# Kernel tuning notes

Hardware: AMD Instinct MI355X
Metric: run time of the kernel (lower is better)

## Reference

```python
import jax, jax.numpy as jnp
import numpy as np

N, E, F, H, C, K = 100000, 1600000, 512, 256, 64, 10
EPS = 1e-5  # BatchNorm1d default eps


def setup_inputs() -> dict:
    key = jax.random.key(0)
    ks = jax.random.split(key, 8)
    x = jax.random.normal(ks[0], (N, F), jnp.float32)
    # edge list with no self-loops (gcn_norm adds the self-loops itself)
    src = jax.random.randint(ks[1], (E,), 0, N)
    off = jax.random.randint(ks[2], (E,), 1, N)
    dst = (src + off) % N
    edge_index = jnp.stack([src, dst])
    s = lambda k, sh: jax.random.normal(k, sh, jnp.float32) * 0.02
    W0 = s(ks[3], (F, H)); b0 = jnp.zeros((H,), jnp.float32)
    g0 = jnp.ones((H,), jnp.float32); be0 = jnp.zeros((H,), jnp.float32)
    W1 = s(ks[4], (H, H)); b1 = jnp.zeros((H,), jnp.float32)
    g1 = jnp.ones((H,), jnp.float32); be1 = jnp.zeros((H,), jnp.float32)
    W2 = s(ks[5], (H, C)); b2 = jnp.zeros((C,), jnp.float32)
    proj_w = s(ks[6], (C, 1)); proj_b = jnp.zeros((1,), jnp.float32)
    return dict(x=x, W0=W0, b0=b0, g0=g0, be0=be0, W1=W1, b1=b1, g1=g1,
                be1=be1, W2=W2, b2=b2, proj_w=proj_w, proj_b=proj_b,
                edge_index=edge_index)


def _batchnorm(h, gamma, beta):
    # training-mode BN over the node (batch) axis, biased variance like torch
    mu = h.mean(0)
    var = h.var(0)
    return gamma * (h - mu) * jax.lax.rsqrt(var + EPS) + beta


def _prop(x, edge_index, proj_w, proj_b):
    n, c = x.shape
    loop = jnp.arange(n, dtype=edge_index.dtype)
    row = jnp.concatenate([edge_index[0], loop])  # message sources (x_j)
    col = jnp.concatenate([edge_index[1], loop])  # aggregation targets
    w = jnp.ones(row.shape, x.dtype)
    deg = jax.ops.segment_sum(w, col, num_segments=n)
    dis = jnp.where(deg > 0, jax.lax.rsqrt(jnp.maximum(deg, 1.0)) * (deg > 0), 0.0)
    dis = jnp.where(deg > 0, deg ** -0.5, 0.0)
    norm = dis[row] * dis[col]  # symmetric GCN normalization per edge

    def hop(xk, _):
        msgs = norm[:, None] * xk[row]               # gather + scale  [E+N, C]
        xk = jax.ops.segment_sum(msgs, col, num_segments=n)  # scatter-add
        return xk, xk

    _, hops = jax.lax.scan(hop, x, None, length=K)   # [K, N, C]
    pps = jnp.concatenate([x[None], hops], axis=0).transpose(1, 0, 2)  # [N, K+1, C]
    score = jax.nn.sigmoid(pps @ proj_w + proj_b)[..., 0]  # [N, K+1]
    return jnp.einsum('nk,nkc->nc', score, pps)      # [N, C]


def reference(x, W0, b0, g0, be0, W1, b1, g1, be1, W2, b2, proj_w, proj_b,
              edge_index):
    h = jax.nn.relu(_batchnorm(x @ W0 + b0, g0, be0))   # dropout is identity (eval)
    h = jax.nn.relu(_batchnorm(h @ W1 + b1, g1, be1))
    h = h @ W2 + b2                                     # [N, C] logits
    out = _prop(h, edge_index, proj_w, proj_b)
    return jax.nn.log_softmax(out, axis=1)
```

## Files before the change

### kernel.cpp

```cpp
#include <hip/hip_runtime.h>
#include <hip/hip_bf16.h>
#include <math.h>

#define NN 100000
#define FF 512
#define HH 256
#define CC 64
#define KHOPS 10
#define BN_EPS 1e-5f

typedef __bf16 bf16x8 __attribute__((ext_vector_type(8)));
typedef float f32x4 __attribute__((ext_vector_type(4)));
typedef unsigned short ushort8v __attribute__((ext_vector_type(8)));

__device__ __forceinline__ unsigned short f2bf(float f) {
    __bf16 b = (__bf16)f;
    return __builtin_bit_cast(unsigned short, b);
}
__device__ __forceinline__ float bf2f(unsigned short h) {
    unsigned u = ((unsigned)h) << 16;
    return __builtin_bit_cast(float, u);
}
__device__ __forceinline__ float lo16(unsigned u) { return bf2f((unsigned short)(u & 0xFFFF)); }
__device__ __forceinline__ float hi16(unsigned u) { return bf2f((unsigned short)(u >> 16)); }
__device__ __forceinline__ unsigned pk(float a, float b) {
    return ((unsigned)f2bf(b) << 16) | (unsigned)f2bf(a);
}

typedef __attribute__((address_space(1))) const void g_void;
typedef __attribute__((address_space(3))) void l_void;
__device__ __forceinline__ void gl2lds16(const void* g, void* l) {
    __builtin_amdgcn_global_load_lds((g_void*)g, (l_void*)l, 16, 0, 0);
}

__global__ void k_zero(float* p, int n) {
    int i = blockIdx.x * blockDim.x + threadIdx.x;
    if (i < n) p[i] = 0.f;
}

__global__ void k_deg_init(int* deg, int n) {
    int i = blockIdx.x * blockDim.x + threadIdx.x;
    if (i < n) deg[i] = 1;
}

__global__ void k_deg_count(const int* __restrict__ dst, int e, int* deg) {
    for (int i = blockIdx.x * blockDim.x + threadIdx.x; i < e; i += gridDim.x * blockDim.x)
        atomicAdd(&deg[dst[i]], 1);
}

__global__ void k_dis(const int* __restrict__ deg, float* dis, int n) {
    int i = blockIdx.x * blockDim.x + threadIdx.x;
    if (i < n) dis[i] = rsqrtf((float)deg[i]);
}

#define SCAN_B 1024
#define SCAN_NB ((NN + SCAN_B - 1) / SCAN_B)

__global__ void k_scan1(const int* __restrict__ deg, int* __restrict__ part, int n) {
    __shared__ int ls[SCAN_B];
    int i = blockIdx.x * SCAN_B + threadIdx.x;
    ls[threadIdx.x] = (i < n) ? deg[i] - 1 : 0;
    __syncthreads();
    for (int d = SCAN_B / 2; d > 0; d >>= 1) {
        if (threadIdx.x < d) ls[threadIdx.x] += ls[threadIdx.x + d];
        __syncthreads();
    }
    if (threadIdx.x == 0) part[blockIdx.x] = ls[0];
}

__global__ void k_scan2(int* part, int* offs_last, int nb) {
    if (threadIdx.x == 0) {
        int run = 0;
        for (int b = 0; b < nb; b++) { int v = part[b]; part[b] = run; run += v; }
        offs_last[0] = run;
    }
}

__global__ void k_scan3(const int* __restrict__ deg, const int* __restrict__ part,
                        int* __restrict__ offs, int* __restrict__ cur, int n) {
    __shared__ int ls[SCAN_B];
    int i = blockIdx.x * SCAN_B + threadIdx.x;
    int v = (i < n) ? deg[i] - 1 : 0;
    ls[threadIdx.x] = v;
    __syncthreads();
    for (int d = 1; d < SCAN_B; d <<= 1) {
        int t = (threadIdx.x >= d) ? ls[threadIdx.x - d] : 0;
        __syncthreads();
        ls[threadIdx.x] += t;
        __syncthreads();
    }
    if (i < n) {
        int ex = part[blockIdx.x] + ls[threadIdx.x] - v;
        offs[i] = ex;
        cur[i] = ex;
    }
}

__global__ void k_fill(const int* __restrict__ src, const int* __restrict__ dst, int e,
                       const float* __restrict__ dis, int* cursor,
                       int* __restrict__ csrc, float* __restrict__ cw) {
    for (int i = blockIdx.x * blockDim.x + threadIdx.x; i < e; i += gridDim.x * blockDim.x) {
        int d = dst[i];
        int s = src[i];
        int p = atomicAdd(&cursor[d], 1);
        csrc[p] = s;
        cw[p] = dis[s] * dis[d];
    }
}

__global__ void k_wt(const float* __restrict__ W, unsigned short* __restrict__ Wt,
                     int K, int N) {
    int i = blockIdx.x * blockDim.x + threadIdx.x;
    if (i < K * N) {
        int n = i / K;
        int k = i - n * K;
        Wt[i] = f2bf(W[(size_t)k * N + n]);
    }
}

template <int AF32, int BN_, int STATS, int NW>
__global__ __launch_bounds__(NW * 64) void k_gemm_mfma(
    const void* __restrict__ Av, const unsigned short* __restrict__ Bt,
    const float* __restrict__ bias, unsigned short* __restrict__ Cb,
    float* __restrict__ sum, float* __restrict__ sumsq,
    int M, int K, int Nd) {
    constexpr int NT = NW * 64;
    constexpr int WC = (NW == 8) ? 4 : 2;
    constexpr int PWN = BN_ / WC;
    constexpr int NREP = PWN / 16;
    constexpr int ACH = AF32 ? 8 : 4;
    constexpr int AOPS = 128 * ACH / NT;
    constexpr int BOPS = BN_ * 4 / NT;
    constexpr int ASZ = AF32 ? 16384 : 8192;
    __shared__ __align__(16) unsigned char Asb[ASZ];
    __shared__ __align__(16) unsigned char Bsb[BN_ * 64];
    const int tid = threadIdx.x;
    const int lane = tid & 63;
    const int wid = tid >> 6;
    const int wrow = wid / WC, wcol = wid % WC;
    const int row_base = blockIdx.y * 128;
    const int col_base = blockIdx.x * BN_;
    const unsigned char* Abase = (const unsigned char*)Av;
    const size_t arowb = (size_t)K * (AF32 ? 4 : 2);

    f32x4 acc[4][NREP];
#pragma unroll
    for (int m = 0; m < 4; m++)
#pragma unroll
        for (int n = 0; n < NREP; n++)
#pragma unroll
            for (int j = 0; j < 4; j++) acc[m][n][j] = 0.f;

    for (int kt = 0; kt < K; kt += 32) {
#pragma unroll
        for (int i = 0; i < AOPS; ++i) {
            int e = i * NT + tid;
            int r = e / ACH;
            int c = e % ACH;
            int cs = AF32 ? (c ^ (r & 7)) : (c ^ ((r >> 1) & 3));
            int grow = row_base + r;
            if (grow > M - 1) grow = M - 1;
            const void* g = Abase + (size_t)grow * arowb + (size_t)kt * (AF32 ? 4 : 2) + (cs << 4);
            gl2lds16(g, Asb + e * 16);
        }
#pragma unroll
        for (int i = 0; i < BOPS; ++i) {
            int e = i * NT + tid;
            int r = e >> 2, c = e & 3;
            int cs = c ^ ((r >> 1) & 3);
            const void* g = (const unsigned char*)Bt + (size_t)(col_base + r) * (K * 2) +
                            (size_t)kt * 2 + (cs << 4);
            gl2lds16(g, Bsb + e * 16);
        }
        __syncthreads();

        bf16x8 af[4], bfr[NREP];
#pragma unroll
        for (int m = 0; m < 4; ++m) {
            int r = wrow * 64 + m * 16 + (lane & 15);
            if (AF32) {
                int x7 = r & 7;
                int q2 = (lane >> 4) * 2;
                f32x4 f0 = *(const f32x4*)(Asb + r * 128 + ((q2 ^ x7) << 4));
                f32x4 f1 = *(const f32x4*)(Asb + r * 128 + (((q2 + 1) ^ x7) << 4));
                bf16x8 a;
                a[0] = (__bf16)f0[0]; a[1] = (__bf16)f0[1]; a[2] = (__bf16)f0[2]; a[3] = (__bf16)f0[3];
                a[4] = (__bf16)f1[0]; a[5] = (__bf16)f1[1]; a[6] = (__bf16)f1[2]; a[7] = (__bf16)f1[3];
                af[m] = a;
            } else {
                int cs = (lane >> 4) ^ ((r >> 1) & 3);
                af[m] = *(const bf16x8*)(Asb + r * 64 + (cs << 4));
            }
        }
#pragma unroll
        for (int n = 0; n < NREP; ++n) {
            int r = wcol * PWN + n * 16 + (lane & 15);
            int cs = (lane >> 4) ^ ((r >> 1) & 3);
            bfr[n] = *(const bf16x8*)(Bsb + r * 64 + (cs << 4));
        }
#pragma unroll
        for (int m = 0; m < 4; ++m)
#pragma unroll
            for (int n = 0; n < NREP; ++n)
                acc[m][n] = __builtin_amdgcn_mfma_f32_16x16x32_bf16(af[m], bfr[n], acc[m][n], 0, 0, 0);
        __syncthreads();
    }

    const int lc = lane & 15;
    const int lr = (lane >> 4) * 4;
#pragma unroll
    for (int m = 0; m < 4; ++m) {
        int gr0 = row_base + wrow * 64 + m * 16 + lr;
#pragma unroll
        for (int n = 0; n < NREP; ++n) {
            int gc = col_base + wcol * PWN + n * 16 + lc;
            float bb = bias[gc];
#pragma unroll
            for (int j = 0; j < 4; ++j) {
                int gr = gr0 + j;
                if (gr < M) Cb[(size_t)gr * Nd + gc] = f2bf(acc[m][n][j] + bb);
            }
        }
    }
    if (STATS) {
#pragma unroll
        for (int n = 0; n < NREP; ++n) {
            int gc = col_base + wcol * PWN + n * 16 + lc;
            float bb = bias[gc];
            float s = 0.f, s2 = 0.f;
#pragma unroll
            for (int m = 0; m < 4; ++m) {
                int gr0 = row_base + wrow * 64 + m * 16 + lr;
#pragma unroll
                for (int j = 0; j < 4; ++j) {
                    if (gr0 + j < M) {
                        float v = acc[m][n][j] + bb;
                        s += v;
                        s2 += v * v;
                    }
                }
            }
            s += __shfl_xor(s, 16); s += __shfl_xor(s, 32);
            s2 += __shfl_xor(s2, 16); s2 += __shfl_xor(s2, 32);
            if ((lane >> 4) == 0) {
                atomicAdd(&sum[gc], s);
                atomicAdd(&sumsq[gc], s2);
            }
        }
    }
}

__global__ void k_bnfin(const float* __restrict__ sum, const float* __restrict__ sq,
                        const float* __restrict__ g, const float* __restrict__ be,
                        float* scale, float* shift) {
    int c = threadIdx.x;
    float mu = sum[c] * (1.f / NN);
    float var = sq[c] * (1.f / NN) - mu * mu;
    float sc = g[c] * rsqrtf(var + BN_EPS);
    scale[c] = sc;
    shift[c] = be[c] - mu * sc;
}

__global__ void k_bnapply(unsigned short* __restrict__ h, const float* __restrict__ scale,
                          const float* __restrict__ shift, int n) {
    int total = n * 32;
    for (int idx = blockIdx.x * blockDim.x + threadIdx.x; idx < total;
         idx += gridDim.x * blockDim.x) {
        int c8 = (idx & 31) * 8;
        ushort8v v = *(ushort8v*)(h + (size_t)idx * 8);
        f32x4 s0 = *(const f32x4*)(scale + c8);
        f32x4 s1 = *(const f32x4*)(scale + c8 + 4);
        f32x4 h0 = *(const f32x4*)(shift + c8);
        f32x4 h1 = *(const f32x4*)(shift + c8 + 4);
#pragma unroll
        for (int j = 0; j < 4; j++) {
            v[j] = f2bf(fmaxf(bf2f(v[j]) * s0[j] + h0[j], 0.f));
            v[j + 4] = f2bf(fmaxf(bf2f(v[j + 4]) * s1[j] + h1[j], 0.f));
        }
        *(ushort8v*)(h + (size_t)idx * 8) = v;
    }
}

__global__ void k_hop(const unsigned short* __restrict__ xin,
                      unsigned short* __restrict__ xout,
                      const int* __restrict__ offs, const int* __restrict__ csrc,
                      const float* __restrict__ cw, const float* __restrict__ dis,
                      int n) {
    int wid = (int)((blockIdx.x * (size_t)blockDim.x + threadIdx.x) >> 6);
    if (wid >= n) return;
    int lane = threadIdx.x & 63;
    int g = lane >> 3;
    int j = lane & 7;
    const uint4* x16 = (const uint4*)xin;
    float y0 = 0.f, y1 = 0.f, y2 = 0.f, y3 = 0.f, y4 = 0.f, y5 = 0.f, y6 = 0.f, y7 = 0.f;
    if (g == 0) {
        float dn = dis[wid];
        float w = dn * dn;
        uint4 v = x16[(size_t)wid * 8 + j];
        y0 = w * lo16(v.x); y1 = w * hi16(v.x);
        y2 = w * lo16(v.y); y3 = w * hi16(v.y);
        y4 = w * lo16(v.z); y5 = w * hi16(v.z);
        y6 = w * lo16(v.w); y7 = w * hi16(v.w);
    }
    int p0 = offs[wid], p1 = offs[wid + 1];
    int p = p0 + g;
    for (; p + 8 < p1; p += 16) {
        int sA = csrc[p], sB = csrc[p + 8];
        float wA = cw[p], wB = cw[p + 8];
        uint4 vA = x16[(size_t)sA * 8 + j];
        uint4 vB = x16[(size_t)sB * 8 + j];
        y0 += wA * lo16(vA.x); y1 += wA * hi16(vA.x);
        y2 += wA * lo16(vA.y); y3 += wA * hi16(vA.y);
        y4 += wA * lo16(vA.z); y5 += wA * hi16(vA.z);
        y6 += wA * lo16(vA.w); y7 += wA * hi16(vA.w);
        y0 += wB * lo16(vB.x); y1 += wB * hi16(vB.x);
        y2 += wB * lo16(vB.y); y3 += wB * hi16(vB.y);
        y4 += wB * lo16(vB.z); y5 += wB * hi16(vB.z);
        y6 += wB * lo16(vB.w); y7 += wB * hi16(vB.w);
    }
    for (; p < p1; p += 8) {
        int s = csrc[p];
        float w = cw[p];
        uint4 v = x16[(size_t)s * 8 + j];
        y0 += w * lo16(v.x); y1 += w * hi16(v.x);
        y2 += w * lo16(v.y); y3 += w * hi16(v.y);
        y4 += w * lo16(v.z); y5 += w * hi16(v.z);
        y6 += w * lo16(v.w); y7 += w * hi16(v.w);
    }
#pragma unroll
    for (int m = 8; m <= 32; m <<= 1) {
        y0 += __shfl_xor(y0, m); y1 += __shfl_xor(y1, m);
        y2 += __shfl_xor(y2, m); y3 += __shfl_xor(y3, m);
        y4 += __shfl_xor(y4, m); y5 += __shfl_xor(y5, m);
        y6 += __shfl_xor(y6, m); y7 += __shfl_xor(y7, m);
    }
    if (g == 0) {
        uint4 r;
        r.x = pk(y0, y1); r.y = pk(y2, y3); r.z = pk(y4, y5); r.w = pk(y6, y7);
        ((uint4*)xout)[(size_t)wid * 8 + j] = r;
    }
}

struct XPack { const unsigned short* p[KHOPS + 1]; };

__global__ void k_finprop(XPack xp, const float* __restrict__ pw,
                          const float* __restrict__ pbp, float* __restrict__ out, int n) {
    int gw = (int)((blockIdx.x * (size_t)blockDim.x + threadIdx.x) >> 6);
    int lane = threadIdx.x & 63;
    int hf = lane >> 5;
    int l = lane & 31;
    int node = gw * 2 + hf;
    if (node >= n) return;
    float pw0 = pw[2 * l], pw1 = pw[2 * l + 1];
    float pb0 = pbp[0];
    float o0 = 0.f, o1 = 0.f;
#pragma unroll
    for (int k = 0; k <= KHOPS; k++) {
        unsigned v = ((const unsigned*)xp.p[k])[(size_t)node * 32 + l];
        float v0 = lo16(v);
        float v1 = hi16(v);
        float d = v0 * pw0 + v1 * pw1;
#pragma unroll
        for (int m = 16; m >= 1; m >>= 1) d += __shfl_xor(d, m);
        float s = 1.f / (1.f + expf(-(d + pb0)));
        o0 += s * v0;
        o1 += s * v1;
    }
    float mx = fmaxf(o0, o1);
#pragma unroll
    for (int m = 16; m >= 1; m >>= 1) mx = fmaxf(mx, __shfl_xor(mx, m));
    float e = expf(o0 - mx) + expf(o1 - mx);
#pragma unroll
    for (int m = 16; m >= 1; m >>= 1) e += __shfl_xor(e, m);
    float lg = mx + logf(e);
    float2 r = make_float2(o0 - lg, o1 - lg);
    *(float2*)(out + (size_t)node * 64 + 2 * l) = r;
}

extern "C" void kernel_launch(void* const* d_in, const int* in_sizes, int n_in,
                              void* d_out, int out_size, void* d_ws, size_t ws_size,
                              hipStream_t stream) {
    const float* x  = (const float*)d_in[0];
    const float* W0 = (const float*)d_in[1];
    const float* b0 = (const float*)d_in[2];
    const float* g0 = (const float*)d_in[3];
    const float* be0 = (const float*)d_in[4];
    const float* W1 = (const float*)d_in[5];
    const float* b1 = (const float*)d_in[6];
    const float* g1 = (const float*)d_in[7];
    const float* be1 = (const float*)d_in[8];
    const float* W2 = (const float*)d_in[9];
    const float* b2 = (const float*)d_in[10];
    const float* pw = (const float*)d_in[11];
    const float* pb = (const float*)d_in[12];
    const int* ei = (const int*)d_in[13];
    const int E = in_sizes[13] / 2;
    const int* esrc = ei;
    const int* edst = ei + E;

    char* ws = (char*)d_ws;
    const size_t XKB = (size_t)NN * CC * 2;
    unsigned short* h0b = (unsigned short*)(ws + 0);
    unsigned short* h1b = (unsigned short*)(ws + 51200000);
    unsigned short* xk[KHOPS + 1];
    xk[0] = (unsigned short*)(ws + 0);
    xk[5] = (unsigned short*)(ws + XKB);
    xk[6] = (unsigned short*)(ws + 2 * XKB);
    xk[7] = (unsigned short*)(ws + 3 * XKB);
    xk[1] = (unsigned short*)(ws + 51200000);
    xk[2] = (unsigned short*)(ws + 51200000 + XKB);
    xk[3] = (unsigned short*)(ws + 51200000 + 2 * XKB);
    xk[4] = (unsigned short*)(ws + 51200000 + 3 * XKB);
    xk[8] = (unsigned short*)(ws + 102400000);
    xk[9] = (unsigned short*)(ws + 115200000);
    xk[10] = (unsigned short*)(ws + 128000000);

    int*   deg  = (int*)  (ws + 140800000);
    float* dis  = (float*)(ws + 141200000);
    int*   offs = (int*)  (ws + 141600000);
    int*   cur  = (int*)  (ws + 142000064);
    int*   csrc = (int*)  (ws + 142400064);
    float* cw   = (float*)(ws + 148800064);
    float* stats = (float*)(ws + 155200064);
    int*   part = (int*)  (ws + 155208256);
    unsigned short* W0t = (unsigned short*)(ws + 155209280);
    unsigned short* W1t = (unsigned short*)(ws + 155471424);
    unsigned short* W2t = (unsigned short*)(ws + 155602496);

    float* sum0 = stats,        *sq0 = stats + 256;
    float* sum1 = stats + 512,  *sq1 = stats + 768;
    float* scale0 = stats + 1024, *shift0 = stats + 1280;
    float* scale1 = stats + 1536, *shift1 = stats + 1792;

    float* out = (float*)d_out;

    const int TPB = 256;
    int ngrid = (NN + TPB - 1) / TPB;
    int egrid = (E + TPB - 1) / TPB;
    int wgrid = (NN * 64 + TPB - 1) / TPB;
    int wgrid2 = (((NN + 1) / 2) * 64 + TPB - 1) / TPB;
    int mtiles = (NN + 127) / 128;

    k_zero<<<2, 1024, 0, stream>>>(stats, 2048);
    k_deg_init<<<ngrid, TPB, 0, stream>>>(deg, NN);
    k_deg_count<<<egrid, TPB, 0, stream>>>(edst, E, deg);
    k_dis<<<ngrid, TPB, 0, stream>>>(deg, dis, NN);
    k_scan1<<<SCAN_NB, SCAN_B, 0, stream>>>(deg, part, NN);
    k_scan2<<<1, 64, 0, stream>>>(part, offs + NN, SCAN_NB);
    k_scan3<<<SCAN_NB, SCAN_B, 0, stream>>>(deg, part, offs, cur, NN);
    k_fill<<<egrid, TPB, 0, stream>>>(esrc, edst, E, dis, cur, csrc, cw);

    k_wt<<<(FF * HH + TPB - 1) / TPB, TPB, 0, stream>>>(W0, W0t, FF, HH);
    k_wt<<<(HH * HH + TPB - 1) / TPB, TPB, 0, stream>>>(W1, W1t, HH, HH);
    k_wt<<<(HH * CC + TPB - 1) / TPB, TPB, 0, stream>>>(W2, W2t, HH, CC);

    k_gemm_mfma<1, 256, 1, 8><<<dim3(1, mtiles), 512, 0, stream>>>(
        x, W0t, b0, h0b, sum0, sq0, NN, FF, HH);
    k_bnfin<<<1, 256, 0, stream>>>(sum0, sq0, g0, be0, scale0, shift0);
    k_bnapply<<<2048, TPB, 0, stream>>>(h0b, scale0, shift0, NN);

    k_gemm_mfma<0, 256, 1, 8><<<dim3(1, mtiles), 512, 0, stream>>>(
        h0b, W1t, b1, h1b, sum1, sq1, NN, HH, HH);
    k_bnfin<<<1, 256, 0, stream>>>(sum1, sq1, g1, be1, scale1, shift1);
    k_bnapply<<<2048, TPB, 0, stream>>>(h1b, scale1, shift1, NN);

    k_gemm_mfma<0, 64, 0, 4><<<dim3(1, mtiles), 256, 0, stream>>>(
        h1b, W2t, b2, xk[0], nullptr, nullptr, NN, HH, CC);

    for (int k = 0; k < KHOPS; k++)
        k_hop<<<wgrid, TPB, 0, stream>>>(xk[k], xk[k + 1], offs, csrc, cw, dis, NN);

    XPack xp;
    for (int k = 0; k <= KHOPS; k++) xp.p[k] = xk[k];
    k_finprop<<<wgrid2, TPB, 0, stream>>>(xp, pw, pb, out, NN);
}
```

Baseline: 887.0 us.

## Fuse BatchNorm apply into next GEMM and load operands directly to registers

Removes the two separate BN+ReLU apply passes by applying scale/shift/ReLU to the A operand inside the following GEMM's load path. The GEMM is also restructured to skip LDS staging: each wave loads its A and B fragments straight from global memory into registers, double-buffered across K steps. This saves two full read-write passes over 100k×256 bf16 activations and the LDS barriers. In exchange, B fragments are reloaded redundantly by every wave and A rows are read without LDS sharing, which may increase global and L2 traffic.

```diff
diff --git a/kernel.cpp b/kernel.cpp
--- a/kernel.cpp
+++ b/kernel.cpp
@@ -25,12 +25,6 @@
 __device__ __forceinline__ float hi16(unsigned u) { return bf2f((unsigned short)(u >> 16)); }
 __device__ __forceinline__ unsigned pk(float a, float b) {
     return ((unsigned)f2bf(b) << 16) | (unsigned)f2bf(a);
-}
-
-typedef __attribute__((address_space(1))) const void g_void;
-typedef __attribute__((address_space(3))) void l_void;
-__device__ __forceinline__ void gl2lds16(const void* g, void* l) {
-    __builtin_amdgcn_global_load_lds((g_void*)g, (l_void*)l, 16, 0, 0);
 }
 
 __global__ void k_zero(float* p, int n) {
@@ -118,102 +112,111 @@
     }
 }
 
-template <int AF32, int BN_, int STATS, int NW>
-__global__ __launch_bounds__(NW * 64) void k_gemm_mfma(
+template <int AF32, int WR, int WC, int STATS, int FUSEBN>
+__global__ __launch_bounds__(WR * WC * 64) void k_gemm_direct(
     const void* __restrict__ Av, const unsigned short* __restrict__ Bt,
     const float* __restrict__ bias, unsigned short* __restrict__ Cb,
+    const float* __restrict__ bnscale, const float* __restrict__ bnshift,
     float* __restrict__ sum, float* __restrict__ sumsq,
     int M, int K, int Nd) {
-    constexpr int NT = NW * 64;
-    constexpr int WC = (NW == 8) ? 4 : 2;
-    constexpr int PWN = BN_ / WC;
-    constexpr int NREP = PWN / 16;
-    constexpr int ACH = AF32 ? 8 : 4;
-    constexpr int AOPS = 128 * ACH / NT;
-    constexpr int BOPS = BN_ * 4 / NT;
-    constexpr int ASZ = AF32 ? 16384 : 8192;
-    __shared__ __align__(16) unsigned char Asb[ASZ];
-    __shared__ __align__(16) unsigned char Bsb[BN_ * 64];
     const int tid = threadIdx.x;
     const int lane = tid & 63;
     const int wid = tid >> 6;
     const int wrow = wid / WC, wcol = wid % WC;
-    const int row_base = blockIdx.y * 128;
-    const int col_base = blockIdx.x * BN_;
-    const unsigned char* Abase = (const unsigned char*)Av;
-    const size_t arowb = (size_t)K * (AF32 ? 4 : 2);
-
-    f32x4 acc[4][NREP];
+    const int row0 = blockIdx.y * (WR * 64) + wrow * 64;
+    const int col0 = wcol * 64;
+    const int rl = lane & 15;
+    const int kl = (lane >> 4) * 8;
+    const float* Af = (const float*)Av;
+    const unsigned short* Ab = (const unsigned short*)Av;
+
+    int arow[4];
+#pragma unroll
+    for (int m = 0; m < 4; ++m) {
+        int r = row0 + m * 16 + rl;
+        arow[m] = (r < M) ? r : (M - 1);
+    }
+
+    f32x4 acc[4][4];
 #pragma unroll
     for (int m = 0; m < 4; m++)
 #pragma unroll
-        for (int n = 0; n < NREP; n++)
+        for (int n = 0; n < 4; n++)
 #pragma unroll
             for (int j = 0; j < 4; j++) acc[m][n][j] = 0.f;
 
-    for (int kt = 0; kt < K; kt += 32) {
-#pragma unroll
-        for (int i = 0; i < AOPS; ++i) {
-            int e = i * NT + tid;
-            int r = e / ACH;
-            int c = e % ACH;
-            int cs = AF32 ? (c ^ (r & 7)) : (c ^ ((r >> 1) & 3));
-            int grow = row_base + r;
-            if (grow > M - 1) grow = M - 1;
-            const void* g = Abase + (size_t)grow * arowb + (size_t)kt * (AF32 ? 4 : 2) + (cs << 4);
-            gl2lds16(g, Asb + e * 16);
-        }
-#pragma unroll
-        for (int i = 0; i < BOPS; ++i) {
-            int e = i * NT + tid;
-            int r = e >> 2, c = e & 3;
-            int cs = c ^ ((r >> 1) & 3);
-            const void* g = (const unsigned char*)Bt + (size_t)(col_base + r) * (K * 2) +
-                            (size_t)kt * 2 + (cs << 4);
-            gl2lds16(g, Bsb + e * 16);
-        }
-        __syncthreads();
-
-        bf16x8 af[4], bfr[NREP];
-#pragma unroll
-        for (int m = 0; m < 4; ++m) {
-            int r = wrow * 64 + m * 16 + (lane & 15);
-            if (AF32) {
-                int x7 = r & 7;
-                int q2 = (lane >> 4) * 2;
-                f32x4 f0 = *(const f32x4*)(Asb + r * 128 + ((q2 ^ x7) << 4));
-                f32x4 f1 = *(const f32x4*)(Asb + r * 128 + (((q2 + 1) ^ x7) << 4));
-                bf16x8 a;
-                a[0] = (__bf16)f0[0]; a[1] = (__bf16)f0[1]; a[2] = (__bf16)f0[2]; a[3] = (__bf16)f0[3];
-                a[4] = (__bf16)f1[0]; a[5] = (__bf16)f1[1]; a[6] = (__bf16)f1[2]; a[7] = (__bf16)f1[3];
-                af[m] = a;
-            } else {
-                int cs = (lane >> 4) ^ ((r >> 1) & 3);
-                af[m] = *(const bf16x8*)(Asb + r * 64 + (cs << 4));
-            }
-        }
-#pragma unroll
-        for (int n = 0; n < NREP; ++n) {
-            int r = wcol * PWN + n * 16 + (lane & 15);
-            int cs = (lane >> 4) ^ ((r >> 1) & 3);
-            bfr[n] = *(const bf16x8*)(Bsb + r * 64 + (cs << 4));
-        }
-#pragma unroll
-        for (int m = 0; m < 4; ++m)
-#pragma unroll
-            for (int n = 0; n < NREP; ++n)
-                acc[m][n] = __builtin_amdgcn_mfma_f32_16x16x32_bf16(af[m], bfr[n], acc[m][n], 0, 0, 0);
-        __syncthreads();
-    }
+    f32x4 rA_[8], rB_[8];
+    bf16x8 aA_[4], aB_[4];
+    bf16x8 bA_[4], bB_[4];
+    f32x4 scA0, scA1, shA0, shA1, scB0, scB1, shB0, shB1;
+
+#define LOADF(kt, rX, aX, bX, sc0, sc1, sh0, sh1)                                   \
+    do {                                                                            \
+        int kc = (kt) + kl;                                                         \
+        if (AF32) {                                                                 \
+            _Pragma("unroll") for (int m = 0; m < 4; ++m) {                         \
+                const float* p = Af + (size_t)arow[m] * K + kc;                     \
+                rX[2 * m] = *(const f32x4*)p;                                       \
+                rX[2 * m + 1] = *(const f32x4*)(p + 4);                             \
+            }                                                                       \
+        } else {                                                                    \
+            _Pragma("unroll") for (int m = 0; m < 4; ++m)                           \
+                aX[m] = *(const bf16x8*)(Ab + (size_t)arow[m] * K + kc);            \
+        }                                                                           \
+        if (FUSEBN) {                                                               \
+            sc0 = *(const f32x4*)(bnscale + kc);                                    \
+            sc1 = *(const f32x4*)(bnscale + kc + 4);                                \
+            sh0 = *(const f32x4*)(bnshift + kc);                                    \
+            sh1 = *(const f32x4*)(bnshift + kc + 4);                                \
+        }                                                                           \
+        _Pragma("unroll") for (int n = 0; n < 4; ++n)                               \
+            bX[n] = *(const bf16x8*)(Bt + (size_t)(col0 + n * 16 + rl) * K + kc);   \
+    } while (0)
+
+#define COMPUTE(rX, aX, bX, sc0, sc1, sh0, sh1)                                     \
+    do {                                                                            \
+        bf16x8 af[4];                                                               \
+        _Pragma("unroll") for (int m = 0; m < 4; ++m) {                             \
+            if (AF32) {                                                             \
+                _Pragma("unroll") for (int j = 0; j < 4; ++j) {                     \
+                    af[m][j] = (__bf16)rX[2 * m][j];                                \
+                    af[m][j + 4] = (__bf16)rX[2 * m + 1][j];                        \
+                }                                                                   \
+            } else if (FUSEBN) {                                                    \
+                _Pragma("unroll") for (int j = 0; j < 4; ++j) {                     \
+                    af[m][j] = (__bf16)fmaxf((float)aX[m][j] * sc0[j] + sh0[j], 0.f);\
+                    af[m][j + 4] =                                                  \
+                        (__bf16)fmaxf((float)aX[m][j + 4] * sc1[j] + sh1[j], 0.f);  \
+                }                                                                   \
+            } else {                                                                \
+                af[m] = aX[m];                                                      \
+            }                                                                       \
+        }                                                                           \
+        _Pragma("unroll") for (int m = 0; m < 4; ++m)                               \
+            _Pragma("unroll") for (int n = 0; n < 4; ++n)                           \
+                acc[m][n] = __builtin_amdgcn_mfma_f32_16x16x32_bf16(                \
+                    af[m], bX[n], acc[m][n], 0, 0, 0);                              \
+    } while (0)
+
+    const int nt = K / 32;
+    LOADF(0, rA_, aA_, bA_, scA0, scA1, shA0, shA1);
+    for (int t = 0; t < nt; t += 2) {
+        if (t + 1 < nt) LOADF((t + 1) * 32, rB_, aB_, bB_, scB0, scB1, shB0, shB1);
+        COMPUTE(rA_, aA_, bA_, scA0, scA1, shA0, shA1);
+        if (t + 2 < nt) LOADF((t + 2) * 32, rA_, aA_, bA_, scA0, scA1, shA0, shA1);
+        if (t + 1 < nt) COMPUTE(rB_, aB_, bB_, scB0, scB1, shB0, shB1);
+    }
+#undef LOADF
+#undef COMPUTE
 
     const int lc = lane & 15;
     const int lr = (lane >> 4) * 4;
 #pragma unroll
     for (int m = 0; m < 4; ++m) {
-        int gr0 = row_base + wrow * 64 + m * 16 + lr;
-#pragma unroll
-        for (int n = 0; n < NREP; ++n) {
-            int gc = col_base + wcol * PWN + n * 16 + lc;
+        int gr0 = row0 + m * 16 + lr;
+#pragma unroll
+        for (int n = 0; n < 4; ++n) {
+            int gc = col0 + n * 16 + lc;
             float bb = bias[gc];
 #pragma unroll
             for (int j = 0; j < 4; ++j) {
@@ -224,13 +227,13 @@
     }
     if (STATS) {
 #pragma unroll
-        for (int n = 0; n < NREP; ++n) {
-            int gc = col_base + wcol * PWN + n * 16 + lc;
+        for (int n = 0; n < 4; ++n) {
+            int gc = col0 + n * 16 + lc;
             float bb = bias[gc];
             float s = 0.f, s2 = 0.f;
 #pragma unroll
             for (int m = 0; m < 4; ++m) {
-                int gr0 = row_base + wrow * 64 + m * 16 + lr;
+                int gr0 = row0 + m * 16 + lr;
 #pragma unroll
                 for (int j = 0; j < 4; ++j) {
                     if (gr0 + j < M) {
@@ -259,26 +262,6 @@
     float sc = g[c] * rsqrtf(var + BN_EPS);
     scale[c] = sc;
     shift[c] = be[c] - mu * sc;
-}
-
-__global__ void k_bnapply(unsigned short* __restrict__ h, const float* __restrict__ scale,
-                          const float* __restrict__ shift, int n) {
-    int total = n * 32;
-    for (int idx = blockIdx.x * blockDim.x + threadIdx.x; idx < total;
-         idx += gridDim.x * blockDim.x) {
-        int c8 = (idx & 31) * 8;
-        ushort8v v = *(ushort8v*)(h + (size_t)idx * 8);
-        f32x4 s0 = *(const f32x4*)(scale + c8);
-        f32x4 s1 = *(const f32x4*)(scale + c8 + 4);
-        f32x4 h0 = *(const f32x4*)(shift + c8);
-        f32x4 h1 = *(const f32x4*)(shift + c8 + 4);
-#pragma unroll
-        for (int j = 0; j < 4; j++) {
-            v[j] = f2bf(fmaxf(bf2f(v[j]) * s0[j] + h0[j], 0.f));
-            v[j + 4] = f2bf(fmaxf(bf2f(v[j + 4]) * s1[j] + h1[j], 0.f));
-        }
-        *(ushort8v*)(h + (size_t)idx * 8) = v;
-    }
 }
 
 __global__ void k_hop(const unsigned short* __restrict__ xin,
@@ -439,7 +422,6 @@
     int egrid = (E + TPB - 1) / TPB;
     int wgrid = (NN * 64 + TPB - 1) / TPB;
     int wgrid2 = (((NN + 1) / 2) * 64 + TPB - 1) / TPB;
-    int mtiles = (NN + 127) / 128;
 
     k_zero<<<2, 1024, 0, stream>>>(stats, 2048);
     k_deg_init<<<ngrid, TPB, 0, stream>>>(deg, NN);
@@ -454,18 +436,16 @@
     k_wt<<<(HH * HH + TPB - 1) / TPB, TPB, 0, stream>>>(W1, W1t, HH, HH);
     k_wt<<<(HH * CC + TPB - 1) / TPB, TPB, 0, stream>>>(W2, W2t, HH, CC);
 
-    k_gemm_mfma<1, 256, 1, 8><<<dim3(1, mtiles), 512, 0, stream>>>(
-        x, W0t, b0, h0b, sum0, sq0, NN, FF, HH);
+    k_gemm_direct<1, 2, 4, 1, 0><<<dim3(1, (NN + 127) / 128), 512, 0, stream>>>(
+        x, W0t, b0, h0b, nullptr, nullptr, sum0, sq0, NN, FF, HH);
     k_bnfin<<<1, 256, 0, stream>>>(sum0, sq0, g0, be0, scale0, shift0);
-    k_bnapply<<<2048, TPB, 0, stream>>>(h0b, scale0, shift0, NN);
-
-    k_gemm_mfma<0, 256, 1, 8><<<dim3(1, mtiles), 512, 0, stream>>>(
-        h0b, W1t, b1, h1b, sum1, sq1, NN, HH, HH);
+
+    k_gemm_direct<0, 2, 4, 1, 1><<<dim3(1, (NN + 127) / 128), 512, 0, stream>>>(
+        h0b, W1t, b1, h1b, scale0, shift0, sum1, sq1, NN, HH, HH);
     k_bnfin<<<1, 256, 0, stream>>>(sum1, sq1, g1, be1, scale1, shift1);
-    k_bnapply<<<2048, TPB, 0, stream>>>(h1b, scale1, shift1, NN);
-
-    k_gemm_mfma<0, 64, 0, 4><<<dim3(1, mtiles), 256, 0, stream>>>(
-        h1b, W2t, b2, xk[0], nullptr, nullptr, NN, HH, CC);
+
+    k_gemm_direct<0, 4, 1, 0, 1><<<dim3(1, (NN + 255) / 256), 256, 0, stream>>>(
+        h1b, W2t, b2, xk[0], scale1, shift1, nullptr, nullptr, NN, HH, CC);
 
     for (int k = 0; k < KHOPS; k++)
         k_hop<<<wgrid, TPB, 0, stream>>>(xk[k], xk[k + 1], offs, csrc, cw, dis, NN);
```

Measured after the change: 1.036 ms. 16.8% more time.
